# Kernel optimization log

Hardware: AMD Instinct MI355X
Metric: run time of the kernel (lower is better)

The kernel has to match this reference:

```python
import jax, jax.numpy as jnp
import numpy as np

B, T, C = 2, 2048, 1024
H, D, R = 16, 64, 32  # heads, head_dim, compression rank (R < D)


def setup_inputs() -> dict:
    key = jax.random.key(0)
    ks = jax.random.split(key, 8)
    s = 0.02
    return {
        "hidden_states": jax.random.normal(ks[0], (B, T, C), jnp.float32),
        "c_attn_w": jax.random.normal(ks[1], (C, 3 * C), jnp.float32) * s,
        "c_attn_b": jnp.zeros((3 * C,), jnp.float32),
        "c_proj_w": jax.random.normal(ks[2], (C, C), jnp.float32) * s,
        "c_proj_b": jnp.zeros((C,), jnp.float32),
        "wk_c": jax.random.normal(ks[3], (D, R), jnp.float32) * (1.0 / np.sqrt(D)),
        "wk_e": jax.random.normal(ks[4], (R, D), jnp.float32) * (1.0 / np.sqrt(R)),
        "wv_c": jax.random.normal(ks[5], (D, R), jnp.float32) * (1.0 / np.sqrt(D)),
        "wv_e": jax.random.normal(ks[6], (R, D), jnp.float32) * (1.0 / np.sqrt(R)),
    }


def reference(hidden_states, c_attn_w, c_attn_b, c_proj_w, c_proj_b,
              wk_c, wk_e, wv_c, wv_e):
    b, t, c = hidden_states.shape
    # GPT2 Conv1D: x @ W + b, then split into Q, K, V
    qkv = hidden_states @ c_attn_w + c_attn_b  # [B,T,3C]
    q, k, v = jnp.split(qkv, 3, axis=-1)

    def split_heads(x):  # [B,T,C] -> [B,H,T,D]
        return x.reshape(b, t, H, D).transpose(0, 2, 1, 3)

    q = split_heads(q)
    k = split_heads(k)
    v = split_heads(v)

    # Low-rank KV compression then expansion (rank R < D path)
    k_lat = jnp.einsum('bhtd,dr->bhtr', k, wk_c)  # [B,H,T,R]
    v_lat = jnp.einsum('bhtd,dr->bhtr', v, wv_c)
    k_exp = jnp.einsum('bhtr,rd->bhtd', k_lat, wk_e)  # [B,H,T,D]
    v_exp = jnp.einsum('bhtr,rd->bhtd', v_lat, wv_e)

    # Causal SDPA (attention_mask is None and q_len > 1 -> is_causal=True)
    scale = 1.0 / np.sqrt(D).astype(np.float32)
    scores = jnp.einsum('bhqd,bhkd->bhqk', q, k_exp) * scale  # [B,H,T,T]
    causal = jnp.tril(jnp.ones((t, t), dtype=bool))
    scores = jnp.where(causal[None, None], scores, jnp.finfo(scores.dtype).min)
    probs = jax.nn.softmax(scores, axis=-1)
    attn = jnp.einsum('bhqk,bhkd->bhqd', probs, v_exp)  # [B,H,T,D]

    # Merge heads and output projection
    attn = attn.transpose(0, 2, 1, 3).reshape(b, t, c)
    out = attn @ c_proj_w + c_proj_b
    return out
```

## Files before the change

### kernel.cpp

```cpp
#include <hip/hip_runtime.h>
#include <cstddef>

typedef __attribute__((ext_vector_type(8))) __bf16 bf16x8;
typedef __attribute__((ext_vector_type(4))) float f32x4;
typedef unsigned short u16;
typedef unsigned int   u32;

#define SCLF (0.125f * 1.44269504f)

__device__ __forceinline__ u16 f2bf(float f){
  union { float f; u32 u; } v; v.f = f;
  u32 r = v.u + 0x7FFFu + ((v.u >> 16) & 1u);
  return (u16)(r >> 16);
}
__device__ __forceinline__ u32 cvtpk(float lo, float hi){
  u32 r; asm("v_cvt_pk_bf16_f32 %0, %1, %2" : "=v"(r) : "v"(lo), "v"(hi)); return r;
}
__device__ __forceinline__ void gll16(const void* g, void* l){
  __builtin_amdgcn_global_load_lds((__attribute__((address_space(1))) void*)g,
                                   (__attribute__((address_space(3))) void*)l, 16, 0, 0);
}

__global__ __launch_bounds__(256) void prep_x(const float* __restrict__ x,
      const float* __restrict__ ba, const float* __restrict__ kc,
      const float* __restrict__ ke, const float* __restrict__ vc,
      u16* __restrict__ Xb, float* __restrict__ b2){
  __shared__ float SH[3104];
  const int bid = blockIdx.x, tid = threadIdx.x;
  if (bid < 1024){
    int i0 = bid*1024 + tid;
    #pragma unroll
    for (int t=0;t<4;++t){
      int i = i0 + t*256;
      float4 v = ((const float4*)x)[i];
      uint2 r; r.x = cvtpk(v.x, v.y); r.y = cvtpk(v.z, v.w);
      ((uint2*)Xb)[i] = r;
    }
  } else {
    const int part = bid - 1024;
    float* BaL = SH;
    float* W65 = SH + 1024;
    *(float4*)&BaL[tid*4] = *(const float4*)&ba[part*1024 + tid*4];
    {
      const float* msrc = (part==0) ? ke : (part==1) ? kc : vc;
      #pragma unroll
      for (int i=0;i<8;++i){
        int idx = tid + i*256;
        float v = msrc[idx];
        int r, d;
        if (part == 0){ r = idx >> 6; d = idx & 63; }
        else          { d = idx >> 5; r = idx & 31; }
        W65[r*65 + d] = v;
      }
    }
    __syncthreads();
    const float scl = (part==0) ? SCLF : 1.f;
    #pragma unroll
    for (int t=0;t<2;++t){
      int l = tid + t*256;
      int hh = l >> 5, r = l & 31;
      float acc = 0.f;
      for (int d=0;d<64;++d) acc += BaL[hh*64 + d] * W65[r*65 + d];
      b2[part*512 + l] = acc * scl;
    }
  }
}

__global__ __launch_bounds__(256) void fold_f32(const float* __restrict__ Wa,
      const float* __restrict__ Wp, const float* __restrict__ kc,
      const float* __restrict__ ke, const float* __restrict__ vc,
      const float* __restrict__ ve, u16* __restrict__ Wt, u16* __restrict__ W2t){
  __shared__ __align__(16) char PS[28928];
  float* SH = (float*)PS;
  u16* As = (u16*)(PS + 16640);
  u16* Bs = (u16*)(PS + 16640 + 8192);
  const int cc = blockIdx.x, y = blockIdx.y;
  const int tid = threadIdx.x;
  const int wv = tid>>6, ln = tid&63;
  const int lr = ln&15, g8 = (ln>>4)*8, gq = ln>>4;
  const int swz = (lr&7)*8;
  const int c0 = cc*64;

  if (y < 48){
    const int ph = y;
    const int part = ph >> 4;
    {
      int r = tid>>3, d8 = tid&7;
      float v[8];
      if (part == 0){
        #pragma unroll
        for (int j=0;j<8;++j) v[j] = ke[r*64 + d8*8 + j]*SCLF;
      } else {
        const float* m = (part==1) ? kc : vc;
        #pragma unroll
        for (int j=0;j<8;++j) v[j] = m[(d8*8+j)*32 + r];
      }
      uint4 w; w.x=cvtpk(v[0],v[1]); w.y=cvtpk(v[2],v[3]); w.z=cvtpk(v[4],v[5]); w.w=cvtpk(v[6],v[7]);
      *(uint4*)&Bs[r*64 + ((d8 ^ (r&7))*8)] = w;
    }
    #pragma unroll
    for (int p=0;p<2;++p){
      int g2 = p*256 + tid;
      int row = g2>>3, gcol = g2&7;
      const float* src = Wa + (size_t)(c0+row)*3072 + ph*64 + gcol*8;
      float4 a = ((const float4*)src)[0], b = ((const float4*)src)[1];
      uint4 w; w.x=cvtpk(a.x,a.y); w.y=cvtpk(a.z,a.w); w.z=cvtpk(b.x,b.y); w.w=cvtpk(b.z,b.w);
      *(uint4*)&As[row*64 + ((gcol ^ (row&7))*8)] = w;
    }
    __syncthreads();
    f32x4 acc[2] = {};
    const int wr = (wv>>1)*32, wn = wv&1;
    #pragma unroll
    for (int ks=0;ks<2;++ks){
      int off = (ks*32 + g8) ^ swz;
      bf16x8 bf = *(const bf16x8*)&Bs[(wn*16+lr)*64 + off];
      #pragma unroll
      for (int mt=0;mt<2;++mt){
        bf16x8 af = *(const bf16x8*)&As[(wr+mt*16+lr)*64 + off];
        acc[mt] = __builtin_amdgcn_mfma_f32_16x16x32_bf16(af, bf, acc[mt], 0,0,0);
      }
    }
    const int n = part*512 + (ph&15)*32 + wn*16 + lr;
    #pragma unroll
    for (int mt=0;mt<2;++mt){
      union { u16 s[4]; uint2 v; } pk;
      #pragma unroll
      for (int r=0;r<4;++r) pk.s[r] = f2bf(acc[mt][r]);
      *(uint2*)&Wt[(size_t)n*1024 + c0 + wr + mt*16 + 4*gq] = pk.v;
    }
  } else {
    const int ph = y - 48;
    {
      int r = tid>>2, c4 = (tid&3)*16;
      const float* src = Wp + (size_t)(ph*64 + r)*1024 + c0 + c4;
      float4 v0 = ((const float4*)src)[0], v1 = ((const float4*)src)[1],
             v2 = ((const float4*)src)[2], v3 = ((const float4*)src)[3];
      float* dst = &SH[r*65 + c4];
      dst[0]=v0.x; dst[1]=v0.y; dst[2]=v0.z; dst[3]=v0.w;
      dst[4]=v1.x; dst[5]=v1.y; dst[6]=v1.z; dst[7]=v1.w;
      dst[8]=v2.x; dst[9]=v2.y; dst[10]=v2.z; dst[11]=v2.w;
      dst[12]=v3.x; dst[13]=v3.y; dst[14]=v3.z; dst[15]=v3.w;
    }
    {
      int r = tid>>3, d8 = tid&7;
      float v[8];
      #pragma unroll
      for (int j=0;j<8;++j) v[j] = ve[r*64 + d8*8 + j];
      uint4 w; w.x=cvtpk(v[0],v[1]); w.y=cvtpk(v[2],v[3]); w.z=cvtpk(v[4],v[5]); w.w=cvtpk(v[6],v[7]);
      *(uint4*)&Bs[r*64 + ((d8 ^ (r&7))*8)] = w;
    }
    __syncthreads();
    #pragma unroll
    for (int p=0;p<2;++p){
      int g2 = p*256 + tid;
      int j = g2>>3, d8 = g2&7;
      float v[8];
      #pragma unroll
      for (int jj=0;jj<8;++jj) v[jj] = SH[(d8*8+jj)*65 + j];
      uint4 w; w.x=cvtpk(v[0],v[1]); w.y=cvtpk(v[2],v[3]); w.z=cvtpk(v[4],v[5]); w.w=cvtpk(v[6],v[7]);
      *(uint4*)&As[j*64 + ((d8 ^ (j&7))*8)] = w;
    }
    __syncthreads();
    f32x4 acc[2] = {};
    const int wr = (wv>>1)*32, wn = wv&1;
    #pragma unroll
    for (int ks=0;ks<2;++ks){
      int off = (ks*32 + g8) ^ swz;
      bf16x8 bf = *(const bf16x8*)&Bs[(wn*16+lr)*64 + off];
      #pragma unroll
      for (int mt=0;mt<2;++mt){
        bf16x8 af = *(const bf16x8*)&As[(wr+mt*16+lr)*64 + off];
        acc[mt] = __builtin_amdgcn_mfma_f32_16x16x32_bf16(af, bf, acc[mt], 0,0,0);
      }
    }
    const int col = ph*32 + wn*16 + lr;
    #pragma unroll
    for (int mt=0;mt<2;++mt)
      #pragma unroll
      for (int r=0;r<4;++r)
        W2t[(size_t)(c0 + wr + mt*16 + 4*gq + r)*512 + col] = f2bf(acc[mt][r]);
  }
}

template<typename OT>
__global__ __launch_bounds__(256) void gemm64(const u16* __restrict__ A, const u16* __restrict__ Bt,
        const float* __restrict__ bias, OT* __restrict__ C, u16* __restrict__ Vt,
        int M, int N, int K, int ldc){
  __shared__ u16 As[64*64];
  __shared__ u16 Bs[128*64];
  const int nwg = gridDim.x * gridDim.y;
  const int id  = blockIdx.x + gridDim.x * blockIdx.y;
  const int nid = (id & 7) * (nwg >> 3) + (id >> 3);
  const int bx = nid % gridDim.x, by = nid / gridDim.x;
  const int tid = threadIdx.x, wv = tid>>6, ln = tid&63;
  const int lr = ln&15, g8 = (ln>>4)*8;
  const int m0 = bx*64, n0 = by*128;
  const int wr = (wv>>1)*32, wc = (wv&1)*64;
  const int lrow = ln>>3, lcol = ((ln&7) ^ lrow)*8;
  const int swz = (lr&7)*8;
  f32x4 acc[2][4] = {};
  const int nk = K >> 6;
  for (int kt=0; kt<nk; ++kt){
    #pragma unroll
    for (int it=0; it<6; ++it){
      int chunk = wv*6 + it;
      if (chunk < 8){
        int row = chunk*8 + lrow;
        gll16(A + (size_t)(m0+row)*K + kt*64 + lcol, &As[chunk*512]);
      } else {
        int bc = chunk - 8;
        int row = bc*8 + lrow;
        gll16(Bt + (size_t)(n0+row)*K + kt*64 + lcol, &Bs[bc*512]);
      }
    }
    __syncthreads();
    #pragma unroll
    for (int ks=0; ks<2; ++ks){
      int off = (ks*32 + g8) ^ swz;
      bf16x8 af[2], bfr[4];
      #pragma unroll
      for (int mt=0;mt<2;++mt) af[mt]  = *(const bf16x8*)&As[(wr+mt*16+lr)*64 + off];
      #pragma unroll
      for (int nt=0;nt<4;++nt) bfr[nt] = *(const bf16x8*)&Bs[(wc+nt*16+lr)*64 + off];
      #pragma unroll
      for (int mt=0;mt<2;++mt)
        #pragma unroll
        for (int nt=0;nt<4;++nt)
          acc[mt][nt] = __builtin_amdgcn_mfma_f32_16x16x32_bf16(af[mt], bfr[nt], acc[mt][nt], 0,0,0);
    }
    __syncthreads();
  }
  if (Vt && n0 >= 1024){
    #pragma unroll
    for (int mt=0;mt<2;++mt){
      int row0 = m0 + wr + mt*16 + 4*(ln>>4);
      int tin  = row0 & 2047;
      int p0 = 4*((tin>>4)&1) + 8*((tin>>2)&3) + 32*(tin>>5);
      size_t vbase = (size_t)(row0 >> 11) * 512;
      #pragma unroll
      for (int nt=0;nt<4;++nt){
        int col = n0 + wc + nt*16 + lr;
        float bv = bias[col];
        int nlat = col - 1024;
        union { u16 s[4]; uint2 v; } pk;
        #pragma unroll
        for (int r=0;r<4;++r) pk.s[r] = f2bf(acc[mt][nt][r] + bv);
        *(uint2*)&Vt[(vbase + nlat)*2048 + p0] = pk.v;
      }
    }
  } else {
    #pragma unroll
    for (int mt=0;mt<2;++mt){
      int row = m0 + wr + mt*16 + 4*(ln>>4);
      #pragma unroll
      for (int nt=0;nt<4;++nt){
        int col = n0 + wc + nt*16 + lr;
        float bv = bias[col];
        #pragma unroll
        for (int r=0;r<4;++r){
          float v = acc[mt][nt][r] + bv;
          if constexpr (sizeof(OT) == 2) C[(size_t)(row+r)*ldc + col] = f2bf(v);
          else                           C[(size_t)(row+r)*ldc + col] = v;
        }
      }
    }
  }
}

__global__ __launch_bounds__(256, 4) void attn_fwd(const u16* __restrict__ QKV,
            const u16* __restrict__ Vt, u16* __restrict__ Out){
  const int bh = blockIdx.x;
  const int y = blockIdx.y;
  const int qt = (y < 8) ? y : (y < 16) ? 23 - y : (y < 24) ? y : 55 - y;
  const int b = bh >> 4, h = bh & 15;
  const int tid = threadIdx.x, wv = tid>>6, ln = tid&63;
  const int sg = wv>>1, wvL = wv&1;
  const int lr = ln&15, gq = ln>>4;
  __shared__ __align__(16) char SMEM[32768];
  u16* KB0 = (u16*)SMEM           + (sg*2    )*2048;
  u16* KB1 = (u16*)SMEM           + (sg*2 + 1)*2048;
  u16* VB0 = (u16*)(SMEM + 16384) + (sg*2    )*2048;
  u16* VB1 = (u16*)(SMEM + 16384) + (sg*2 + 1)*2048;
  const int q0 = qt*64;
  const size_t base = (size_t)(b*2048) * 1536;
  const u16* qrowA = QKV + base + (size_t)(q0 + wvL*32 + lr)*1536 + h*32;
  bf16x8 qfA = *(const bf16x8*)(qrowA + gq*8);
  bf16x8 qfB = *(const bf16x8*)(qrowA + (size_t)16*1536 + gq*8);
  const int qgA = q0 + wvL*32 + lr, qgB = qgA + 16;
  f32x4 oA0 = {}, oA1 = {}, oB0 = {}, oB1 = {};
  float lA = 0.f, lB = 0.f;
  const u16* ksrc = QKV + base + 512 + h*32;
  const u16* vsrc = Vt + (size_t)(bh*32)*2048;

  const int ci = wvL*64 + ln;
  const int rK = ci>>2, cK = 8*((ci&3) ^ (rK&3));
  const int rV = ci>>3, cV = 8*((ci&7) ^ (rV&7));

  int offK[4], offV[2][2];
  #pragma unroll
  for (int nt=0;nt<4;++nt)
    offK[nt] = (nt*16+lr)*64 + ((gq*16) ^ ((lr&3)<<4));
  #pragma unroll
  for (int dt=0;dt<2;++dt)
    #pragma unroll
    for (int c=0;c<2;++c)
      offV[dt][c] = (dt*16+lr)*128 + ((c*64 + gq*16) ^ ((lr&7)<<4));

  if (sg <= qt){
    gll16(ksrc + (size_t)(sg*64 + rK)*1536 + cK,      KB0 + wvL*512);
    gll16(ksrc + (size_t)(sg*64 + 32 + rK)*1536 + cK, KB0 + 1024 + wvL*512);
    gll16(vsrc + (size_t)rV*2048 + sg*64 + cV,        VB0 + wvL*512);
    gll16(vsrc + (size_t)(16+rV)*2048 + sg*64 + cV,   VB0 + 1024 + wvL*512);
  }
  __syncthreads();
  const u16* kpa = ksrc + (size_t)(sg*64 + 128 + rK)*1536 + cK;
  const u16* kpb = ksrc + (size_t)(sg*64 + 160 + rK)*1536 + cK;
  const u16* vpa = vsrc + (size_t)rV*2048 + sg*64 + 128 + cV;
  const u16* vpb = vsrc + (size_t)(16+rV)*2048 + sg*64 + 128 + cV;
  const size_t KSTEP = (size_t)128*1536;

  #define ABODY(II, KBC, VBC, KBN, VBN) do { \
    const int kt = 2*(II) + sg; \
    if (kt + 2 <= qt){ \
      gll16(kpa, (KBN) + wvL*512); \
      gll16(kpb, (KBN) + 1024 + wvL*512); \
      gll16(vpa, (VBN) + wvL*512); \
      gll16(vpb, (VBN) + 1024 + wvL*512); \
      kpa += KSTEP; kpb += KSTEP; vpa += 128; vpb += 128; \
    } \
    if (kt <= qt){ \
      f32x4 sA[4] = {}, sB[4] = {}; \
      __builtin_amdgcn_s_setprio(1); \
      _Pragma("unroll") for (int nt=0;nt<4;++nt){ \
        bf16x8 k0 = *(const bf16x8*)((const char*)(KBC) + offK[nt]); \
        sA[nt] = __builtin_amdgcn_mfma_f32_16x16x32_bf16(k0, qfA, sA[nt], 0,0,0); \
        sB[nt] = __builtin_amdgcn_mfma_f32_16x16x32_bf16(k0, qfB, sB[nt], 0,0,0); \
      } \
      __builtin_amdgcn_s_setprio(0); \
      if (kt == qt){ \
        const int kv0 = kt*64; \
        _Pragma("unroll") for (int nt=0;nt<4;++nt) \
        _Pragma("unroll") for (int r=0;r<4;++r){ \
          int k = kv0 + nt*16 + 4*gq + r; \
          if (k > qgA) sA[nt][r] = -1e30f; \
          if (k > qgB) sB[nt][r] = -1e30f; \
        } \
      } \
      union { u32 u[4]; bf16x8 v; } paA0, paA1, paB0, paB1; \
      { \
        float p0,p1,p2,p3,p4,p5,p6,p7; \
        p0=__builtin_amdgcn_exp2f(sA[0][0]); p1=__builtin_amdgcn_exp2f(sA[0][1]); \
        p2=__builtin_amdgcn_exp2f(sA[0][2]); p3=__builtin_amdgcn_exp2f(sA[0][3]); \
        p4=__builtin_amdgcn_exp2f(sA[1][0]); p5=__builtin_amdgcn_exp2f(sA[1][1]); \
        p6=__builtin_amdgcn_exp2f(sA[1][2]); p7=__builtin_amdgcn_exp2f(sA[1][3]); \
        lA += ((p0+p1)+(p2+p3)) + ((p4+p5)+(p6+p7)); \
        paA0.u[0]=cvtpk(p0,p1); paA0.u[1]=cvtpk(p2,p3); paA0.u[2]=cvtpk(p4,p5); paA0.u[3]=cvtpk(p6,p7); \
        p0=__builtin_amdgcn_exp2f(sA[2][0]); p1=__builtin_amdgcn_exp2f(sA[2][1]); \
        p2=__builtin_amdgcn_exp2f(sA[2][2]); p3=__builtin_amdgcn_exp2f(sA[2][3]); \
        p4=__builtin_amdgcn_exp2f(sA[3][0]); p5=__builtin_amdgcn_exp2f(sA[3][1]); \
        p6=__builtin_amdgcn_exp2f(sA[3][2]); p7=__builtin_amdgcn_exp2f(sA[3][3]); \
        lA += ((p0+p1)+(p2+p3)) + ((p4+p5)+(p6+p7)); \
        paA1.u[0]=cvtpk(p0,p1); paA1.u[1]=cvtpk(p2,p3); paA1.u[2]=cvtpk(p4,p5); paA1.u[3]=cvtpk(p6,p7); \
        p0=__builtin_amdgcn_exp2f(sB[0][0]); p1=__builtin_amdgcn_exp2f(sB[0][1]); \
        p2=__builtin_amdgcn_exp2f(sB[0][2]); p3=__builtin_amdgcn_exp2f(sB[0][3]); \
        p4=__builtin_amdgcn_exp2f(sB[1][0]); p5=__builtin_amdgcn_exp2f(sB[1][1]); \
        p6=__builtin_amdgcn_exp2f(sB[1][2]); p7=__builtin_amdgcn_exp2f(sB[1][3]); \
        lB += ((p0+p1)+(p2+p3)) + ((p4+p5)+(p6+p7)); \
        paB0.u[0]=cvtpk(p0,p1); paB0.u[1]=cvtpk(p2,p3); paB0.u[2]=cvtpk(p4,p5); paB0.u[3]=cvtpk(p6,p7); \
        p0=__builtin_amdgcn_exp2f(sB[2][0]); p1=__builtin_amdgcn_exp2f(sB[2][1]); \
        p2=__builtin_amdgcn_exp2f(sB[2][2]); p3=__builtin_amdgcn_exp2f(sB[2][3]); \
        p4=__builtin_amdgcn_exp2f(sB[3][0]); p5=__builtin_amdgcn_exp2f(sB[3][1]); \
        p6=__builtin_amdgcn_exp2f(sB[3][2]); p7=__builtin_amdgcn_exp2f(sB[3][3]); \
        lB += ((p0+p1)+(p2+p3)) + ((p4+p5)+(p6+p7)); \
        paB1.u[0]=cvtpk(p0,p1); paB1.u[1]=cvtpk(p2,p3); paB1.u[2]=cvtpk(p4,p5); paB1.u[3]=cvtpk(p6,p7); \
      } \
      __builtin_amdgcn_s_setprio(1); \
      { \
        bf16x8 v00 = *(const bf16x8*)((const char*)(VBC) + offV[0][0]); \
        bf16x8 v10 = *(const bf16x8*)((const char*)(VBC) + offV[1][0]); \
        bf16x8 v01 = *(const bf16x8*)((const char*)(VBC) + offV[0][1]); \
        bf16x8 v11 = *(const bf16x8*)((const char*)(VBC) + offV[1][1]); \
        oA0 = __builtin_amdgcn_mfma_f32_16x16x32_bf16(paA0.v, v00, oA0, 0,0,0); \
        oA1 = __builtin_amdgcn_mfma_f32_16x16x32_bf16(paA0.v, v10, oA1, 0,0,0); \
        oB0 = __builtin_amdgcn_mfma_f32_16x16x32_bf16(paB0.v, v00, oB0, 0,0,0); \
        oB1 = __builtin_amdgcn_mfma_f32_16x16x32_bf16(paB0.v, v10, oB1, 0,0,0); \
        oA0 = __builtin_amdgcn_mfma_f32_16x16x32_bf16(paA1.v, v01, oA0, 0,0,0); \
        oA1 = __builtin_amdgcn_mfma_f32_16x16x32_bf16(paA1.v, v11, oA1, 0,0,0); \
        oB0 = __builtin_amdgcn_mfma_f32_16x16x32_bf16(paB1.v, v01, oB0, 0,0,0); \
        oB1 = __builtin_amdgcn_mfma_f32_16x16x32_bf16(paB1.v, v11, oB1, 0,0,0); \
      } \
      __builtin_amdgcn_s_setprio(0); \
    } \
    __syncthreads(); \
  } while(0)

  const int nmax = (qt + 2) >> 1;
  const int jmax = (nmax + 1) >> 1;
  for (int j = 0; j < jmax; ++j){
    ABODY(2*j,   KB0, VB0, KB1, VB1);
    ABODY(2*j+1, KB1, VB1, KB0, VB0);
  }
  lA += __shfl_xor(lA, 16); lA += __shfl_xor(lA, 32);
  lB += __shfl_xor(lB, 16); lB += __shfl_xor(lB, 32);

  float* MO = (float*)SMEM;
  float* ML = (float*)(SMEM + 12288);
  if (sg == 1){
    #pragma unroll
    for (int r=0;r<4;++r){
      int rowA = wvL*32 + 4*gq + r;
      MO[rowA*34 + lr]            = oA0[r];
      MO[rowA*34 + 16 + lr]       = oA1[r];
      MO[(rowA+16)*34 + lr]       = oB0[r];
      MO[(rowA+16)*34 + 16 + lr]  = oB1[r];
    }
    if (gq == 0){ ML[wvL*32 + lr] = lA; ML[wvL*32 + 16 + lr] = lB; }
  }
  __syncthreads();
  if (sg == 0){
    float lSA = lA + ML[wvL*32 + lr];
    float lSB = lB + ML[wvL*32 + 16 + lr];
    float lA_o[4], lB_o[4];
    #pragma unroll
    for (int r=0;r<4;++r){ lA_o[r] = __shfl(lSA, 4*gq + r); lB_o[r] = __shfl(lSB, 4*gq + r); }
    #pragma unroll
    for (int r=0;r<4;++r){
      int rowA = wvL*32 + 4*gq + r;
      float vA0 = (oA0[r] + MO[rowA*34 + lr])           / lA_o[r];
      float vA1 = (oA1[r] + MO[rowA*34 + 16 + lr])      / lA_o[r];
      float vB0 = (oB0[r] + MO[(rowA+16)*34 + lr])      / lB_o[r];
      float vB1 = (oB1[r] + MO[(rowA+16)*34 + 16 + lr]) / lB_o[r];
      size_t obA = (size_t)(b*2048 + q0 + rowA)*512 + h*32;
      Out[obA + lr]      = f2bf(vA0);
      Out[obA + 16 + lr] = f2bf(vA1);
      size_t obB = obA + (size_t)16*512;
      Out[obB + lr]      = f2bf(vB0);
      Out[obB + 16 + lr] = f2bf(vB1);
    }
  }
}

#define WS_B2   0u
#define WS_WT   8192u
#define WS_W2T  (WS_WT + 3145728u)
#define WS_XB   (WS_W2T + 1048576u)
#define WS_QKV  (WS_XB + 8388608u)
#define WS_VT   (WS_QKV + 12582912u)
#define WS_ATT  (WS_VT + 4194304u)

extern "C" void kernel_launch(void* const* d_in, const int* in_sizes, int n_in,
                              void* d_out, int out_size, void* d_ws, size_t ws_size,
                              hipStream_t stream) {
  const float* x  = (const float*)d_in[0];
  const float* Wa = (const float*)d_in[1];
  const float* ba = (const float*)d_in[2];
  const float* Wp = (const float*)d_in[3];
  const float* bp = (const float*)d_in[4];
  const float* kc = (const float*)d_in[5];
  const float* ke = (const float*)d_in[6];
  const float* vc = (const float*)d_in[7];
  const float* ve = (const float*)d_in[8];
  float* out = (float*)d_out;
  char* ws = (char*)d_ws;
  float* b2  = (float*)(ws + WS_B2);
  u16* Wt    = (u16*)(ws + WS_WT);
  u16* W2t   = (u16*)(ws + WS_W2T);
  u16* Xb    = (u16*)(ws + WS_XB);
  u16* QKVb  = (u16*)(ws + WS_QKV);
  u16* Vt    = (u16*)(ws + WS_VT);
  u16* Att   = (u16*)(ws + WS_ATT);

  prep_x<<<1027, 256, 0, stream>>>(x, ba, kc, ke, vc, Xb, b2);
  fold_f32<<<dim3(16,64), 256, 0, stream>>>(Wa, Wp, kc, ke, vc, ve, Wt, W2t);
  gemm64<u16><<<dim3(64,12), 256, 0, stream>>>(Xb, Wt, b2, QKVb, Vt, 4096, 1536, 1024, 1536);
  attn_fwd<<<dim3(32,32), 256, 0, stream>>>(QKVb, Vt, Att);
  gemm64<float><<<dim3(64,8), 256, 0, stream>>>(Att, W2t, bp, out, (u16*)nullptr, 4096, 1024, 512, 1024);
}
```

Baseline: 69.34 us.

## Triple-buffer K/V tiles in attention with explicit vmcnt waits and reversed tile order

Moves the attention kernel from double- to triple-buffered LDS staging of K/V tiles, prefetching two tiles ahead. Explicit s_waitcnt vmcnt plus raw s_barrier replace __syncthreads so outstanding loads can stay in flight across iterations. The query-tile schedule changes from a zigzag mapping to longest-first ordering. Shared memory grows to 48KB and launch bounds drop from 4 to 3 blocks per CU, which lowers occupancy.

```diff
diff --git a/kernel.cpp b/kernel.cpp
--- a/kernel.cpp
+++ b/kernel.cpp
@@ -20,6 +20,9 @@
   __builtin_amdgcn_global_load_lds((__attribute__((address_space(1))) void*)g,
                                    (__attribute__((address_space(3))) void*)l, 16, 0, 0);
 }
+#define BARRIER() asm volatile("s_barrier" ::: "memory")
+#define WAITV4()  asm volatile("s_waitcnt vmcnt(4)" ::: "memory")
+#define WAITV0()  asm volatile("s_waitcnt vmcnt(0)" ::: "memory")
 
 __global__ __launch_bounds__(256) void prep_x(const float* __restrict__ x,
       const float* __restrict__ ba, const float* __restrict__ kc,
@@ -267,20 +270,21 @@
   }
 }
 
-__global__ __launch_bounds__(256, 4) void attn_fwd(const u16* __restrict__ QKV,
+__global__ __launch_bounds__(256, 3) void attn_fwd(const u16* __restrict__ QKV,
             const u16* __restrict__ Vt, u16* __restrict__ Out){
   const int bh = blockIdx.x;
-  const int y = blockIdx.y;
-  const int qt = (y < 8) ? y : (y < 16) ? 23 - y : (y < 24) ? y : 55 - y;
+  const int qt = 31 - blockIdx.y;
   const int b = bh >> 4, h = bh & 15;
   const int tid = threadIdx.x, wv = tid>>6, ln = tid&63;
   const int sg = wv>>1, wvL = wv&1;
   const int lr = ln&15, gq = ln>>4;
-  __shared__ __align__(16) char SMEM[32768];
-  u16* KB0 = (u16*)SMEM           + (sg*2    )*2048;
-  u16* KB1 = (u16*)SMEM           + (sg*2 + 1)*2048;
-  u16* VB0 = (u16*)(SMEM + 16384) + (sg*2    )*2048;
-  u16* VB1 = (u16*)(SMEM + 16384) + (sg*2 + 1)*2048;
+  __shared__ __align__(16) char SMEM[49152];
+  u16* KB0 = (u16*)(SMEM)         + (sg*3 + 0)*2048;
+  u16* KB1 = (u16*)(SMEM)         + (sg*3 + 1)*2048;
+  u16* KB2 = (u16*)(SMEM)         + (sg*3 + 2)*2048;
+  u16* VB0 = (u16*)(SMEM + 24576) + (sg*3 + 0)*2048;
+  u16* VB1 = (u16*)(SMEM + 24576) + (sg*3 + 1)*2048;
+  u16* VB2 = (u16*)(SMEM + 24576) + (sg*3 + 2)*2048;
   const int q0 = qt*64;
   const size_t base = (size_t)(b*2048) * 1536;
   const u16* qrowA = QKV + base + (size_t)(q0 + wvL*32 + lr)*1536 + h*32;
@@ -306,28 +310,28 @@
     for (int c=0;c<2;++c)
       offV[dt][c] = (dt*16+lr)*128 + ((c*64 + gq*16) ^ ((lr&7)<<4));
 
-  if (sg <= qt){
-    gll16(ksrc + (size_t)(sg*64 + rK)*1536 + cK,      KB0 + wvL*512);
-    gll16(ksrc + (size_t)(sg*64 + 32 + rK)*1536 + cK, KB0 + 1024 + wvL*512);
-    gll16(vsrc + (size_t)rV*2048 + sg*64 + cV,        VB0 + wvL*512);
-    gll16(vsrc + (size_t)(16+rV)*2048 + sg*64 + cV,   VB0 + 1024 + wvL*512);
-  }
-  __syncthreads();
-  const u16* kpa = ksrc + (size_t)(sg*64 + 128 + rK)*1536 + cK;
-  const u16* kpb = ksrc + (size_t)(sg*64 + 160 + rK)*1536 + cK;
-  const u16* vpa = vsrc + (size_t)rV*2048 + sg*64 + 128 + cV;
-  const u16* vpb = vsrc + (size_t)(16+rV)*2048 + sg*64 + 128 + cV;
+  const u16* kpa = ksrc + (size_t)(sg*64 + rK)*1536 + cK;
+  const u16* kpb = ksrc + (size_t)(sg*64 + 32 + rK)*1536 + cK;
+  const u16* vpa = vsrc + (size_t)rV*2048 + sg*64 + cV;
+  const u16* vpb = vsrc + (size_t)(16+rV)*2048 + sg*64 + cV;
   const size_t KSTEP = (size_t)128*1536;
+
+  #define STG3(KBN, VBN) do { \
+    gll16(kpa, (KBN) + wvL*512); \
+    gll16(kpb, (KBN) + 1024 + wvL*512); \
+    gll16(vpa, (VBN) + wvL*512); \
+    gll16(vpb, (VBN) + 1024 + wvL*512); \
+    kpa += KSTEP; kpb += KSTEP; vpa += 128; vpb += 128; \
+  } while(0)
+
+  if (sg <= qt)      STG3(KB0, VB0);
+  if (sg + 2 <= qt){ STG3(KB1, VB1); WAITV4(); } else { WAITV0(); }
+  BARRIER();
 
   #define ABODY(II, KBC, VBC, KBN, VBN) do { \
     const int kt = 2*(II) + sg; \
-    if (kt + 2 <= qt){ \
-      gll16(kpa, (KBN) + wvL*512); \
-      gll16(kpb, (KBN) + 1024 + wvL*512); \
-      gll16(vpa, (VBN) + wvL*512); \
-      gll16(vpb, (VBN) + 1024 + wvL*512); \
-      kpa += KSTEP; kpb += KSTEP; vpa += 128; vpb += 128; \
-    } \
+    const bool stg = (kt + 4 <= qt); \
+    if (stg) STG3(KBN, VBN); \
     if (kt <= qt){ \
       f32x4 sA[4] = {}, sB[4] = {}; \
       __builtin_amdgcn_s_setprio(1); \
@@ -391,14 +395,16 @@
       } \
       __builtin_amdgcn_s_setprio(0); \
     } \
-    __syncthreads(); \
+    if (stg) WAITV4(); else WAITV0(); \
+    BARRIER(); \
   } while(0)
 
   const int nmax = (qt + 2) >> 1;
-  const int jmax = (nmax + 1) >> 1;
+  const int jmax = (nmax + 2) / 3;
   for (int j = 0; j < jmax; ++j){
-    ABODY(2*j,   KB0, VB0, KB1, VB1);
-    ABODY(2*j+1, KB1, VB1, KB0, VB0);
+    ABODY(3*j+0, KB0, VB0, KB2, VB2);
+    ABODY(3*j+1, KB1, VB1, KB0, VB0);
+    ABODY(3*j+2, KB2, VB2, KB1, VB1);
   }
   lA += __shfl_xor(lA, 16); lA += __shfl_xor(lA, 32);
   lB += __shfl_xor(lB, 16); lB += __shfl_xor(lB, 32);
```

Result: no change. 69.33 us (median of 3 runs) (-0.0%).
